# Performance work log

Measured on AMD Instinct MI355X. Metric: run time of the kernel, lower is better.

## Reference

```python
import jax, jax.numpy as jnp
import numpy as np

HEADS = 16
DK = 64
THETA = 10000.0


def _rope(x, cos, sin):
    # x: (B, S, H, dk) -> rotate consecutive pairs as complex numbers
    xr = x.reshape(*x.shape[:-1], -1, 2)
    a, b = xr[..., 0], xr[..., 1]
    c = cos[None, :, None, :]  # (1, S, 1, dk//2)
    s = sin[None, :, None, :]
    out = jnp.stack([a * c - b * s, a * s + b * c], axis=-1)
    return out.reshape(x.shape)


def setup_inputs() -> dict:
    key = jax.random.key(0)
    ks = jax.random.split(key, 5)
    B, S, D = 4, 2048, 1024
    x = jax.random.normal(ks[0], (B, S, D), dtype=jnp.float32)
    scale = 1.0 / np.sqrt(D).astype(np.float32)
    Wq = jax.random.normal(ks[1], (D, D), dtype=jnp.float32) * scale
    Wk = jax.random.normal(ks[2], (D, D), dtype=jnp.float32) * scale
    Wv = jax.random.normal(ks[3], (D, D), dtype=jnp.float32) * scale
    Wo = jax.random.normal(ks[4], (D, D), dtype=jnp.float32) * scale
    # freqs_cis = exp(i * t * theta^{-2j/dk}), represented as cos/sin
    t = jnp.arange(S, dtype=jnp.float32)
    inv_freq = 1.0 / (THETA ** (jnp.arange(0, DK, 2, dtype=jnp.float32) / DK))
    ang = t[:, None] * inv_freq[None, :]  # (S, dk//2)
    return {"in_features": x, "freqs_cos": jnp.cos(ang), "freqs_sin": jnp.sin(ang),
            "Wq": Wq, "Wk": Wk, "Wv": Wv, "Wo": Wo}


def reference(in_features, freqs_cos, freqs_sin, Wq, Wk, Wv, Wo):
    B, S, D = in_features.shape
    H = HEADS
    dk = D // H
    # Linear projections (torch Linear: x @ W.T)
    q = (in_features @ Wq.T).reshape(B, S, H, dk)
    k = (in_features @ Wk.T).reshape(B, S, H, dk)
    v = (in_features @ Wv.T).reshape(B, S, H, dk)
    q = _rope(q, freqs_cos, freqs_sin)
    k = _rope(k, freqs_cos, freqs_sin)
    scale = 1.0 / jnp.sqrt(jnp.asarray(dk, dtype=q.dtype))
    scores = jnp.einsum("bqhd,bkhd->bhqk", q, k) * scale
    mask = jnp.tril(jnp.ones((S, S), dtype=bool))
    scores = jnp.where(mask[None, None, :, :], scores, -jnp.inf)
    attn = jax.nn.softmax(scores, axis=-1)
    out = jnp.einsum("bhqk,bkhd->bqhd", attn, v).reshape(B, S, D)
    return out @ Wo.T
```

## Files before the change

kernel.cpp:

```cpp
#include <hip/hip_runtime.h>
#include <hip/hip_bf16.h>

typedef __attribute__((ext_vector_type(8))) __bf16 bf16x8;
typedef __attribute__((ext_vector_type(4))) __bf16 bf16x4;
typedef __attribute__((ext_vector_type(4))) float f32x4;
typedef __attribute__((ext_vector_type(2))) unsigned int u32x2;

static __device__ __forceinline__ f32x4 mfma_bf16(bf16x8 a, bf16x8 b, f32x4 c) {
  return __builtin_amdgcn_mfma_f32_16x16x32_bf16(a, b, c, 0, 0, 0);
}

static __device__ __forceinline__ void gload_lds16(const void* g, void* l) {
  __builtin_amdgcn_global_load_lds(
      (__attribute__((address_space(1))) unsigned int*)g,
      (__attribute__((address_space(3))) unsigned int*)l, 16, 0, 0);
}

static __device__ __forceinline__ unsigned int cvt_pk_bf16(float lo, float hi) {
  unsigned int r;
  asm volatile("v_cvt_pk_bf16_f32 %0, %1, %2" : "=v"(r) : "v"(lo), "v"(hi));
  return r;
}

__global__ void cvt_bf16(const float* __restrict__ in, __bf16* __restrict__ out, int n4) {
  int i = blockIdx.x * blockDim.x + threadIdx.x;
  if (i >= n4) return;
  f32x4 v = ((const f32x4*)in)[i];
  bf16x4 o;
#pragma unroll
  for (int k = 0; k < 4; ++k) o[k] = (__bf16)v[k];
  ((bf16x4*)out)[i] = o;
}

__global__ void cvt_w4(const float* __restrict__ w0, const float* __restrict__ w1,
                       const float* __restrict__ w2, const float* __restrict__ w3,
                       __bf16* __restrict__ o0, __bf16* __restrict__ o1,
                       __bf16* __restrict__ o2, __bf16* __restrict__ o3) {
  const float* in; __bf16* out;
  switch (blockIdx.y) {
    case 0: in = w0; out = o0; break;
    case 1: in = w1; out = o1; break;
    case 2: in = w2; out = o2; break;
    default: in = w3; out = o3; break;
  }
  int i = blockIdx.x * blockDim.x + threadIdx.x;
  f32x4 v = ((const f32x4*)in)[i];
  bf16x4 o;
#pragma unroll
  for (int k = 0; k < 4; ++k) o[k] = (__bf16)v[k];
  ((bf16x4*)out)[i] = o;
}

#define ISSUE_A(kt, slot)                                                   \
  {                                                                         \
    const int k0 = (kt) * 64;                                               \
    __bf16* d = Al + (slot) * 16384 + t * 8;                                \
    gload_lds16(Ag + k0, d);                                                \
    gload_lds16(Ag + (size_t)64 * K + k0, d + 4096);                        \
    gload_lds16(Ag + (size_t)128 * K + k0, d + 8192);                       \
    gload_lds16(Ag + (size_t)192 * K + k0, d + 12288);                      \
  }
#define ISSUE_B(kt, slot)                                                   \
  {                                                                         \
    const int k0 = (kt) * 64;                                               \
    __bf16* d = Bl + (slot) * 8192 + t * 8;                                 \
    gload_lds16(Wg + k0, d);                                                \
    gload_lds16(Wg + (size_t)64 * K + k0, d + 4096);                        \
  }

#define GEMM_PIPELINE                                                       \
  constexpr int K = 1024;                                                   \
  constexpr int NT = K / 64;                                                \
  extern __shared__ __align__(16) __bf16 dynlds[];                          \
  __bf16* Al = dynlds;                                                      \
  __bf16* Bl = dynlds + 49152;                                              \
  const int t = threadIdx.x;                                                \
  const int lane = t & 63, wave = t >> 6;                                   \
  const int g = lane >> 4, ln = lane & 15;                                  \
  const int wm = wave >> 1, wn = wave & 1;                                  \
  f32x4 acc[4][4] = {};                                                     \
  const int srow8 = t >> 3;                                                 \
  const int scole = (((t & 7) ^ ((t >> 3) & 7)) << 3);                      \
  const __bf16* Ag = A + (size_t)(bm * 256 + srow8) * K + scole;            \
  const __bf16* Wg = W + (size_t)(bn * 128 + srow8) * K + scole;            \
  const int axr = ln & 7;                                                   \
  int aoff[4], boff[4];                                                     \
  _Pragma("unroll") for (int i = 0; i < 4; ++i)                             \
    aoff[i] = (wm * 64 + i * 16 + ln) * 64;                                 \
  _Pragma("unroll") for (int j = 0; j < 4; ++j)                             \
    boff[j] = (wn * 64 + j * 16 + ln) * 64;                                 \
  ISSUE_B(0, 0); ISSUE_A(0, 0); ISSUE_A(1, 1);                              \
  asm volatile("s_waitcnt vmcnt(4)" ::: "memory");                          \
  __builtin_amdgcn_s_barrier();                                             \
  int sa = 0;                                                               \
  for (int tt = 0; tt < NT; ++tt) {                                         \
    const __bf16* Ab = Al + sa * 16384;                                     \
    const __bf16* Bb = Bl + (tt & 1) * 8192;                                \
    bf16x8 af[4], bf[4];                                                    \
    _Pragma("unroll") for (int i = 0; i < 4; ++i)                           \
      af[i] = *(const bf16x8*)(Ab + aoff[i] + ((g ^ axr) << 3));            \
    _Pragma("unroll") for (int j = 0; j < 4; ++j)                           \
      bf[j] = *(const bf16x8*)(Bb + boff[j] + ((g ^ axr) << 3));            \
    if (tt + 1 < NT) ISSUE_B(tt + 1, (tt + 1) & 1);                         \
    if (tt + 2 < NT) ISSUE_A(tt + 2, sa == 0 ? 2 : sa - 1);                 \
    __builtin_amdgcn_s_barrier();                                           \
    asm volatile("s_waitcnt lgkmcnt(0)" ::: "memory");                      \
    __builtin_amdgcn_sched_barrier(0);                                      \
    __builtin_amdgcn_s_setprio(1);                                          \
    _Pragma("unroll") for (int i = 0; i < 4; ++i)                           \
      _Pragma("unroll") for (int j = 0; j < 4; ++j)                         \
        acc[i][j] = mfma_bf16(af[i], bf[j], acc[i][j]);                     \
    __builtin_amdgcn_s_setprio(0);                                          \
    __builtin_amdgcn_s_barrier();                                           \
    _Pragma("unroll") for (int i = 0; i < 4; ++i)                           \
      af[i] = *(const bf16x8*)(Ab + aoff[i] + (((4 | g) ^ axr) << 3));      \
    _Pragma("unroll") for (int j = 0; j < 4; ++j)                           \
      bf[j] = *(const bf16x8*)(Bb + boff[j] + (((4 | g) ^ axr) << 3));      \
    if (tt < NT - 2) { asm volatile("s_waitcnt vmcnt(4)" ::: "memory"); }   \
    else             { asm volatile("s_waitcnt vmcnt(0)" ::: "memory"); }   \
    __builtin_amdgcn_s_barrier();                                           \
    asm volatile("s_waitcnt lgkmcnt(0)" ::: "memory");                      \
    __builtin_amdgcn_sched_barrier(0);                                      \
    __builtin_amdgcn_s_setprio(1);                                          \
    _Pragma("unroll") for (int i = 0; i < 4; ++i)                           \
      _Pragma("unroll") for (int j = 0; j < 4; ++j)                         \
        acc[i][j] = mfma_bf16(af[i], bf[j], acc[i][j]);                     \
    __builtin_amdgcn_s_setprio(0);                                          \
    __builtin_amdgcn_s_barrier();                                           \
    sa = (sa == 2) ? 0 : sa + 1;                                            \
  }

template <int MODE>
__global__ __launch_bounds__(512, 1)
void gemm256(const __bf16* __restrict__ A, const __bf16* __restrict__ W,
             void* __restrict__ outp,
             const float* __restrict__ fcos, const float* __restrict__ fsin) {
  const int lin = blockIdx.x + blockIdx.y * 8;
  const int bm = (lin & 7) + 8 * ((lin >> 3) & 3);
  const int bn = lin >> 5;

  GEMM_PIPELINE

#pragma unroll
  for (int i = 0; i < 4; ++i) {
    const int mbase = bm * 256 + wm * 64 + i * 16 + g * 4;
#pragma unroll
    for (int j = 0; j < 4; ++j) {
      const int col = bn * 128 + wn * 64 + j * 16 + ln;
      if constexpr (MODE == 0 || MODE == 1) {
        const int fi = (col & 63) >> 1;
        const bool odd = (col & 1) != 0;
        __bf16* O = (__bf16*)outp;
#pragma unroll
        for (int r = 0; r < 4; ++r) {
          const int row = mbase + r;
          const int tok = row & 2047;
          const float cs = fcos[tok * 32 + fi];
          const float sn = fsin[tok * 32 + fi];
          const float own = acc[i][j][r];
          const float oth = __shfl_xor(own, 1);
          float val = own * cs + (odd ? oth * sn : -oth * sn);
          if constexpr (MODE == 0) val *= 0.1803368802f;
          O[(size_t)row * 1024 + col] = (__bf16)val;
        }
      } else if constexpr (MODE == 2) {
        __bf16* O = (__bf16*)outp;
        const int bb = mbase >> 11;
        const int tok = mbase & 2047;
        bf16x4 pk;
#pragma unroll
        for (int r = 0; r < 4; ++r) pk[r] = (__bf16)acc[i][j][r];
        *(bf16x4*)(O + ((size_t)(bb * 1024 + col)) * 2048 + tok) = pk;
      } else {
        float* O = (float*)outp;
#pragma unroll
        for (int r = 0; r < 4; ++r)
          O[(size_t)(mbase + r) * 1024 + col] = acc[i][j][r];
      }
    }
  }
}

static __device__ __forceinline__ void sm_pack_pv(
    f32x4* sa, float& m, float& l, f32x4* o,
    unsigned int* Pw, const __bf16* Vb, const int g, const int ln) {
  const float a0 = fmaxf(fmaxf(sa[0][0], sa[0][1]), sa[0][2]);
  const float a1 = fmaxf(fmaxf(sa[0][3], sa[1][0]), sa[1][1]);
  const float a2 = fmaxf(fmaxf(sa[1][2], sa[1][3]), sa[2][0]);
  const float a3 = fmaxf(fmaxf(sa[2][1], sa[2][2]), sa[2][3]);
  const float a4 = fmaxf(fmaxf(sa[3][0], sa[3][1]), sa[3][2]);
  float pm = fmaxf(fmaxf(fmaxf(a0, a1), a2), fmaxf(fmaxf(a3, a4), sa[3][3]));

  if (__any(pm > m + 8.f)) {
    pm = fmaxf(pm, __shfl_xor(pm, 16));
    pm = fmaxf(pm, __shfl_xor(pm, 32));
    const float mn = fmaxf(m, pm);
    const float alpha = exp2f(m - mn);
    m = mn;
    l *= alpha;
#pragma unroll
    for (int c2 = 0; c2 < 4; ++c2)
#pragma unroll
      for (int r = 0; r < 4; ++r) o[c2][r] *= alpha;
  }

  float p[4][4];
#pragma unroll
  for (int c = 0; c < 4; ++c)
#pragma unroll
    for (int r = 0; r < 4; ++r) p[c][r] = exp2f(sa[c][r] - m);

  float ts[8];
#pragma unroll
  for (int i = 0; i < 8; ++i) ts[i] = p[i >> 2][i & 3] + p[2 + (i >> 2)][i & 3];
#pragma unroll
  for (int st = 4; st >= 1; st >>= 1)
#pragma unroll
    for (int i = 0; i < st; ++i) ts[i] += ts[i + st];
  float rs = ts[0];
  rs += __shfl_xor(rs, 16);
  rs += __shfl_xor(rs, 32);
  l += rs;

  unsigned int* Pr = Pw + ln * 36;
#pragma unroll
  for (int c = 0; c < 4; ++c) {
    u32x2 w;
    w[0] = cvt_pk_bf16(p[c][0], p[c][1]);
    w[1] = cvt_pk_bf16(p[c][2], p[c][3]);
    *(u32x2*)(Pr + 8 * c + 2 * g) = w;
  }

  const int axr = ln & 7;
  __builtin_amdgcn_s_setprio(1);
#pragma unroll
  for (int sh = 0; sh < 2; ++sh) {
    bf16x8 pb = *(const bf16x8*)((const __bf16*)Pw + ln * 72 + sh * 32 + g * 8);
#pragma unroll
    for (int c2 = 0; c2 < 4; ++c2) {
      bf16x8 vf = *(const bf16x8*)(Vb + (c2 * 16 + ln) * 64 +
                                   (((sh * 4 + g) ^ axr) << 3));
      o[c2] = mfma_bf16(vf, pb, o[c2]);
    }
  }
  __builtin_amdgcn_s_setprio(0);
}

__global__ __launch_bounds__(512, 6)
void attn_fwd(const __bf16* __restrict__ Q, const __bf16* __restrict__ Kk,
              const __bf16* __restrict__ Vt, __bf16* __restrict__ U) {
  constexpr int S = 2048;
  __shared__ __align__(16) __bf16 Klds[2][64 * 64];
  __shared__ __align__(16) __bf16 Vlds[2][64 * 64];
  __shared__ __align__(16) unsigned int Plds[8][16 * 36];

  const int t = threadIdx.x;
  const int lane = t & 63, wave = t >> 6;
  const int g = lane >> 4, ln = lane & 15;
  const int lin = blockIdx.x + blockIdx.y * 16;
  const int bh = (lin & 7) * 8 + ((lin >> 3) & 7);
  const int qt = 15 - (lin >> 6);
  const int b = bh >> 4, h = bh & 15;
  const int q0 = qt * 128;
  const int nt = 2 * qt + 2;

  const __bf16* Qb = Q + ((size_t)(b * S + q0 + wave * 16 + ln)) * 1024 + h * 64;
  bf16x8 qf0 = *(const bf16x8*)(Qb + g * 8);
  bf16x8 qf1 = *(const bf16x8*)(Qb + 32 + g * 8);

  f32x4 o[4] = {};
  float mrow = -3.0e38f, lrow = 0.f;

  const int srow = t >> 3;
  const int schunk = ((t & 7) ^ (srow & 7)) * 8;
  const __bf16* Kg = Kk + ((size_t)(b * S + srow)) * 1024 + h * 64 + schunk;
  const __bf16* Vg = Vt + ((size_t)(b * 1024 + h * 64 + srow)) * 2048 + schunk;

  gload_lds16(Kg, (__bf16*)Klds[0] + t * 8);
  gload_lds16(Vg, (__bf16*)Vlds[0] + t * 8);
  __syncthreads();

  const int axr = ln & 7;
  for (int kt = 0; kt < nt; ++kt) {
    const int cur = kt & 1;
    if (kt + 1 < nt) {
      gload_lds16(Kg + (size_t)(kt + 1) * 64 * 1024, (__bf16*)Klds[cur ^ 1] + t * 8);
      gload_lds16(Vg + (kt + 1) * 64, (__bf16*)Vlds[cur ^ 1] + t * 8);
    }
    const int kv0 = kt * 64;

    f32x4 sa[4] = {};
    __builtin_amdgcn_s_setprio(1);
#pragma unroll
    for (int s = 0; s < 2; ++s) {
      const bf16x8 qf = s ? qf1 : qf0;
#pragma unroll
      for (int c = 0; c < 4; ++c) {
        bf16x8 kf = *(const bf16x8*)(Klds[cur] + (c * 16 + ln) * 64 +
                                     (((s * 4 + g) ^ axr) << 3));
        sa[c] = mfma_bf16(kf, qf, sa[c]);
      }
    }
    __builtin_amdgcn_s_setprio(0);

    const int rfbase = q0 + wave * 16;
    const int rq = rfbase + ln;
    if (kv0 + 63 > rfbase) {
#pragma unroll
      for (int c = 0; c < 4; ++c)
#pragma unroll
        for (int r = 0; r < 4; ++r)
          if (kv0 + c * 16 + g * 4 + r > rq) sa[c][r] = -1e30f;
    }

    sm_pack_pv(sa, mrow, lrow, o, Plds[wave], Vlds[cur], g, ln);
    __syncthreads();
  }

  const float rl = 1.0f / lrow;
  __bf16* Ub = U + ((size_t)(b * S + q0 + wave * 16 + ln)) * 1024 + h * 64;
#pragma unroll
  for (int c2 = 0; c2 < 4; ++c2) {
    bf16x4 pk4;
#pragma unroll
    for (int r = 0; r < 4; ++r) pk4[r] = (__bf16)(o[c2][r] * rl);
    *(bf16x4*)(Ub + 16 * c2 + 4 * g) = pk4;
  }
}

extern "C" void kernel_launch(void* const* d_in, const int* in_sizes, int n_in,
                              void* d_out, int out_size, void* d_ws, size_t ws_size,
                              hipStream_t stream) {
  const float* x    = (const float*)d_in[0];
  const float* fcos = (const float*)d_in[1];
  const float* fsin = (const float*)d_in[2];
  const float* Wq   = (const float*)d_in[3];
  const float* Wk   = (const float*)d_in[4];
  const float* Wv   = (const float*)d_in[5];
  const float* Wo   = (const float*)d_in[6];

  char* ws = (char*)d_ws;
  __bf16* xb  = (__bf16*)(ws);
  __bf16* Wqb = (__bf16*)(ws + (16u << 20));
  __bf16* Wkb = (__bf16*)(ws + (18u << 20));
  __bf16* Wvb = (__bf16*)(ws + (20u << 20));
  __bf16* Wob = (__bf16*)(ws + (22u << 20));
  __bf16* Qb  = (__bf16*)(ws + (24u << 20));
  __bf16* Kb  = (__bf16*)(ws + (40u << 20));
  __bf16* Vtb = (__bf16*)(ws + (56u << 20));
  __bf16* Ub  = xb;

  cvt_bf16<<<8192, 256, 0, stream>>>(x, xb, 8192 * 1024 / 4);
  cvt_w4<<<dim3(1024, 4), 256, 0, stream>>>(Wq, Wk, Wv, Wo, Wqb, Wkb, Wvb, Wob);

  dim3 gg(8, 32);
  const size_t lds = 131072;
  gemm256<0><<<gg, 512, lds, stream>>>(xb, Wqb, Qb,  fcos, fsin);
  gemm256<1><<<gg, 512, lds, stream>>>(xb, Wkb, Kb,  fcos, fsin);
  gemm256<2><<<gg, 512, lds, stream>>>(xb, Wvb, Vtb, nullptr, nullptr);
  attn_fwd<<<dim3(16, 64), 512, 0, stream>>>(Qb, Kb, Vtb, Ub);
  gemm256<3><<<gg, 512, lds, stream>>>(Ub, Wob, d_out, nullptr, nullptr);
}
```

Baseline: 180.3 us.

## Process 128-key tiles in attention with register-staged prefetch; fuse conversion kernels

The attention kernel now handles 128 keys per iteration instead of 64. The next K/V tile is prefetched into registers through ordinary global loads, replacing direct-to-LDS double buffering, and written to a single LDS buffer after a barrier. The causal mask is applied only on the last tile. This halves the number of loop iterations and barriers per key, at the cost of more registers, an extra barrier per iteration, and no LDS double buffering. The two fp32-to-bf16 conversion kernels are merged into one launch to save launch overhead.

```diff
diff --git a/kernel.cpp b/kernel.cpp
--- a/kernel.cpp
+++ b/kernel.cpp
@@ -22,28 +22,29 @@
   return r;
 }
 
-__global__ void cvt_bf16(const float* __restrict__ in, __bf16* __restrict__ out, int n4) {
-  int i = blockIdx.x * blockDim.x + threadIdx.x;
-  if (i >= n4) return;
-  f32x4 v = ((const f32x4*)in)[i];
-  bf16x4 o;
-#pragma unroll
-  for (int k = 0; k < 4; ++k) o[k] = (__bf16)v[k];
-  ((bf16x4*)out)[i] = o;
-}
-
-__global__ void cvt_w4(const float* __restrict__ w0, const float* __restrict__ w1,
-                       const float* __restrict__ w2, const float* __restrict__ w3,
-                       __bf16* __restrict__ o0, __bf16* __restrict__ o1,
-                       __bf16* __restrict__ o2, __bf16* __restrict__ o3) {
-  const float* in; __bf16* out;
-  switch (blockIdx.y) {
-    case 0: in = w0; out = o0; break;
-    case 1: in = w1; out = o1; break;
-    case 2: in = w2; out = o2; break;
-    default: in = w3; out = o3; break;
-  }
-  int i = blockIdx.x * blockDim.x + threadIdx.x;
+__global__ void cvt_all(const float* __restrict__ x,
+                        const float* __restrict__ w0, const float* __restrict__ w1,
+                        const float* __restrict__ w2, const float* __restrict__ w3,
+                        __bf16* __restrict__ xo,
+                        __bf16* __restrict__ o0, __bf16* __restrict__ o1,
+                        __bf16* __restrict__ o2, __bf16* __restrict__ o3) {
+  const int blk = blockIdx.x;
+  const float* in;
+  __bf16* out;
+  int base;
+  if (blk < 8192) {
+    in = x; out = xo; base = blk;
+  } else {
+    const int wi = (blk - 8192) >> 10;
+    base = (blk - 8192) & 1023;
+    switch (wi) {
+      case 0: in = w0; out = o0; break;
+      case 1: in = w1; out = o1; break;
+      case 2: in = w2; out = o2; break;
+      default: in = w3; out = o3; break;
+    }
+  }
+  const int i = base * 256 + threadIdx.x;
   f32x4 v = ((const f32x4*)in)[i];
   bf16x4 o;
 #pragma unroll
@@ -181,77 +182,12 @@
   }
 }
 
-static __device__ __forceinline__ void sm_pack_pv(
-    f32x4* sa, float& m, float& l, f32x4* o,
-    unsigned int* Pw, const __bf16* Vb, const int g, const int ln) {
-  const float a0 = fmaxf(fmaxf(sa[0][0], sa[0][1]), sa[0][2]);
-  const float a1 = fmaxf(fmaxf(sa[0][3], sa[1][0]), sa[1][1]);
-  const float a2 = fmaxf(fmaxf(sa[1][2], sa[1][3]), sa[2][0]);
-  const float a3 = fmaxf(fmaxf(sa[2][1], sa[2][2]), sa[2][3]);
-  const float a4 = fmaxf(fmaxf(sa[3][0], sa[3][1]), sa[3][2]);
-  float pm = fmaxf(fmaxf(fmaxf(a0, a1), a2), fmaxf(fmaxf(a3, a4), sa[3][3]));
-
-  if (__any(pm > m + 8.f)) {
-    pm = fmaxf(pm, __shfl_xor(pm, 16));
-    pm = fmaxf(pm, __shfl_xor(pm, 32));
-    const float mn = fmaxf(m, pm);
-    const float alpha = exp2f(m - mn);
-    m = mn;
-    l *= alpha;
-#pragma unroll
-    for (int c2 = 0; c2 < 4; ++c2)
-#pragma unroll
-      for (int r = 0; r < 4; ++r) o[c2][r] *= alpha;
-  }
-
-  float p[4][4];
-#pragma unroll
-  for (int c = 0; c < 4; ++c)
-#pragma unroll
-    for (int r = 0; r < 4; ++r) p[c][r] = exp2f(sa[c][r] - m);
-
-  float ts[8];
-#pragma unroll
-  for (int i = 0; i < 8; ++i) ts[i] = p[i >> 2][i & 3] + p[2 + (i >> 2)][i & 3];
-#pragma unroll
-  for (int st = 4; st >= 1; st >>= 1)
-#pragma unroll
-    for (int i = 0; i < st; ++i) ts[i] += ts[i + st];
-  float rs = ts[0];
-  rs += __shfl_xor(rs, 16);
-  rs += __shfl_xor(rs, 32);
-  l += rs;
-
-  unsigned int* Pr = Pw + ln * 36;
-#pragma unroll
-  for (int c = 0; c < 4; ++c) {
-    u32x2 w;
-    w[0] = cvt_pk_bf16(p[c][0], p[c][1]);
-    w[1] = cvt_pk_bf16(p[c][2], p[c][3]);
-    *(u32x2*)(Pr + 8 * c + 2 * g) = w;
-  }
-
-  const int axr = ln & 7;
-  __builtin_amdgcn_s_setprio(1);
-#pragma unroll
-  for (int sh = 0; sh < 2; ++sh) {
-    bf16x8 pb = *(const bf16x8*)((const __bf16*)Pw + ln * 72 + sh * 32 + g * 8);
-#pragma unroll
-    for (int c2 = 0; c2 < 4; ++c2) {
-      bf16x8 vf = *(const bf16x8*)(Vb + (c2 * 16 + ln) * 64 +
-                                   (((sh * 4 + g) ^ axr) << 3));
-      o[c2] = mfma_bf16(vf, pb, o[c2]);
-    }
-  }
-  __builtin_amdgcn_s_setprio(0);
-}
-
 __global__ __launch_bounds__(512, 6)
 void attn_fwd(const __bf16* __restrict__ Q, const __bf16* __restrict__ Kk,
               const __bf16* __restrict__ Vt, __bf16* __restrict__ U) {
   constexpr int S = 2048;
-  __shared__ __align__(16) __bf16 Klds[2][64 * 64];
-  __shared__ __align__(16) __bf16 Vlds[2][64 * 64];
+  __shared__ __align__(16) __bf16 Klds[128 * 64];
+  __shared__ __align__(16) __bf16 Vlds[64 * 128];
   __shared__ __align__(16) unsigned int Plds[8][16 * 36];
 
   const int t = threadIdx.x;
@@ -262,7 +198,7 @@
   const int qt = 15 - (lin >> 6);
   const int b = bh >> 4, h = bh & 15;
   const int q0 = qt * 128;
-  const int nt = 2 * qt + 2;
+  const int nt2 = qt + 1;
 
   const __bf16* Qb = Q + ((size_t)(b * S + q0 + wave * 16 + ln)) * 1024 + h * 64;
   bf16x8 qf0 = *(const bf16x8*)(Qb + g * 8);
@@ -271,49 +207,135 @@
   f32x4 o[4] = {};
   float mrow = -3.0e38f, lrow = 0.f;
 
-  const int srow = t >> 3;
-  const int schunk = ((t & 7) ^ (srow & 7)) * 8;
-  const __bf16* Kg = Kk + ((size_t)(b * S + srow)) * 1024 + h * 64 + schunk;
-  const __bf16* Vg = Vt + ((size_t)(b * 1024 + h * 64 + srow)) * 2048 + schunk;
-
-  gload_lds16(Kg, (__bf16*)Klds[0] + t * 8);
-  gload_lds16(Vg, (__bf16*)Vlds[0] + t * 8);
+  const int rkK = t >> 2;
+  const int cK0 = (t & 3) * 2;
+  const int rdV = t >> 3;
+  const int cV0 = (t & 7) * 2;
+  const __bf16* KgRow = Kk + ((size_t)(b * S + rkK)) * 1024 + h * 64;
+  const __bf16* VgRow = Vt + ((size_t)(b * 1024 + h * 64 + rdV)) * 2048;
+  const int okA = (cK0 ^ (rkK & 7)) * 8;
+  const int okB = ((cK0 + 1) ^ (rkK & 7)) * 8;
+  const int ovA = ((cV0 >> 3) * 64) + (((cV0 & 7) ^ (rdV & 7)) * 8);
+  const int ovB = (((cV0 + 1) >> 3) * 64) + ((((cV0 + 1) & 7) ^ (rdV & 7)) * 8);
+  __bf16* KwA = Klds + rkK * 64 + cK0 * 8;
+  __bf16* VwA = Vlds + rdV * 128 + cV0 * 8;
+
+  {
+    bf16x8 ka = *(const bf16x8*)(KgRow + okA);
+    bf16x8 kb2 = *(const bf16x8*)(KgRow + okB);
+    bf16x8 va = *(const bf16x8*)(VgRow + ovA);
+    bf16x8 vb2 = *(const bf16x8*)(VgRow + ovB);
+    *(bf16x8*)KwA = ka;
+    *(bf16x8*)(KwA + 8) = kb2;
+    *(bf16x8*)VwA = va;
+    *(bf16x8*)(VwA + 8) = vb2;
+  }
   __syncthreads();
 
   const int axr = ln & 7;
-  for (int kt = 0; kt < nt; ++kt) {
-    const int cur = kt & 1;
-    if (kt + 1 < nt) {
-      gload_lds16(Kg + (size_t)(kt + 1) * 64 * 1024, (__bf16*)Klds[cur ^ 1] + t * 8);
-      gload_lds16(Vg + (kt + 1) * 64, (__bf16*)Vlds[cur ^ 1] + t * 8);
-    }
-    const int kv0 = kt * 64;
-
-    f32x4 sa[4] = {};
+  const int rq = q0 + wave * 16 + ln;
+  for (int kt2 = 0; kt2 < nt2; ++kt2) {
+    bf16x8 ka, kb2, va, vb2;
+    if (kt2 + 1 < nt2) {
+      const size_t kadv = (size_t)(kt2 + 1) * 128 * 1024;
+      const int vadv = (kt2 + 1) * 128;
+      ka = *(const bf16x8*)(KgRow + kadv + okA);
+      kb2 = *(const bf16x8*)(KgRow + kadv + okB);
+      va = *(const bf16x8*)(VgRow + vadv + ovA);
+      vb2 = *(const bf16x8*)(VgRow + vadv + ovB);
+    }
+    const int kv0 = kt2 * 128;
+
+    f32x4 sa[8] = {};
     __builtin_amdgcn_s_setprio(1);
 #pragma unroll
     for (int s = 0; s < 2; ++s) {
       const bf16x8 qf = s ? qf1 : qf0;
 #pragma unroll
-      for (int c = 0; c < 4; ++c) {
-        bf16x8 kf = *(const bf16x8*)(Klds[cur] + (c * 16 + ln) * 64 +
+      for (int c = 0; c < 8; ++c) {
+        bf16x8 kf = *(const bf16x8*)(Klds + (c * 16 + ln) * 64 +
                                      (((s * 4 + g) ^ axr) << 3));
         sa[c] = mfma_bf16(kf, qf, sa[c]);
       }
     }
     __builtin_amdgcn_s_setprio(0);
 
-    const int rfbase = q0 + wave * 16;
-    const int rq = rfbase + ln;
-    if (kv0 + 63 > rfbase) {
-#pragma unroll
-      for (int c = 0; c < 4; ++c)
+    if (kt2 == nt2 - 1) {
+#pragma unroll
+      for (int c = 0; c < 8; ++c)
 #pragma unroll
         for (int r = 0; r < 4; ++r)
           if (kv0 + c * 16 + g * 4 + r > rq) sa[c][r] = -1e30f;
     }
 
-    sm_pack_pv(sa, mrow, lrow, o, Plds[wave], Vlds[cur], g, ln);
+    float tmax[8];
+#pragma unroll
+    for (int c = 0; c < 8; ++c)
+      tmax[c] = fmaxf(fmaxf(sa[c][0], sa[c][1]), fmaxf(sa[c][2], sa[c][3]));
+#pragma unroll
+    for (int c = 0; c < 4; ++c) tmax[c] = fmaxf(tmax[c], tmax[c + 4]);
+    float pm = fmaxf(fmaxf(tmax[0], tmax[1]), fmaxf(tmax[2], tmax[3]));
+
+    if (__any(pm > mrow + 8.f)) {
+      pm = fmaxf(pm, __shfl_xor(pm, 16));
+      pm = fmaxf(pm, __shfl_xor(pm, 32));
+      const float mn = fmaxf(mrow, pm);
+      const float alpha = exp2f(mrow - mn);
+      mrow = mn;
+      lrow *= alpha;
+#pragma unroll
+      for (int c2 = 0; c2 < 4; ++c2)
+#pragma unroll
+        for (int r = 0; r < 4; ++r) o[c2][r] *= alpha;
+    }
+
+    float p[8][4];
+#pragma unroll
+    for (int c = 0; c < 8; ++c)
+#pragma unroll
+      for (int r = 0; r < 4; ++r) p[c][r] = exp2f(sa[c][r] - mrow);
+
+    float ts[8];
+#pragma unroll
+    for (int c = 0; c < 8; ++c) ts[c] = (p[c][0] + p[c][1]) + (p[c][2] + p[c][3]);
+#pragma unroll
+    for (int c = 0; c < 4; ++c) ts[c] += ts[c + 4];
+    float rs = (ts[0] + ts[1]) + (ts[2] + ts[3]);
+    rs += __shfl_xor(rs, 16);
+    rs += __shfl_xor(rs, 32);
+    lrow += rs;
+
+    unsigned int* Pr = Plds[wave] + ln * 36;
+#pragma unroll
+    for (int h2 = 0; h2 < 2; ++h2) {
+#pragma unroll
+      for (int c = 0; c < 4; ++c) {
+        u32x2 w;
+        w[0] = cvt_pk_bf16(p[h2 * 4 + c][0], p[h2 * 4 + c][1]);
+        w[1] = cvt_pk_bf16(p[h2 * 4 + c][2], p[h2 * 4 + c][3]);
+        *(u32x2*)(Pr + 8 * c + 2 * g) = w;
+      }
+      __builtin_amdgcn_s_setprio(1);
+#pragma unroll
+      for (int sh = 0; sh < 2; ++sh) {
+        bf16x8 pb = *(const bf16x8*)((const __bf16*)Plds[wave] + ln * 72 + sh * 32 + g * 8);
+#pragma unroll
+        for (int c2 = 0; c2 < 4; ++c2) {
+          bf16x8 vf = *(const bf16x8*)(Vlds + (c2 * 16 + ln) * 128 + h2 * 64 +
+                                       (((sh * 4 + g) ^ axr) << 3));
+          o[c2] = mfma_bf16(vf, pb, o[c2]);
+        }
+      }
+      __builtin_amdgcn_s_setprio(0);
+    }
+
+    __syncthreads();
+    if (kt2 + 1 < nt2) {
+      *(bf16x8*)KwA = ka;
+      *(bf16x8*)(KwA + 8) = kb2;
+      *(bf16x8*)VwA = va;
+      *(bf16x8*)(VwA + 8) = vb2;
+    }
     __syncthreads();
   }
 
@@ -350,8 +372,7 @@
   __bf16* Vtb = (__bf16*)(ws + (56u << 20));
   __bf16* Ub  = xb;
 
-  cvt_bf16<<<8192, 256, 0, stream>>>(x, xb, 8192 * 1024 / 4);
-  cvt_w4<<<dim3(1024, 4), 256, 0, stream>>>(Wq, Wk, Wv, Wo, Wqb, Wkb, Wvb, Wob);
+  cvt_all<<<12288, 256, 0, stream>>>(x, Wq, Wk, Wv, Wo, xb, Wqb, Wkb, Wvb, Wob);
 
   dim3 gg(8, 32);
   const size_t lds = 131072;
```

Result: slower. 304.6 us (+69.0%).
